# Optimization experiments

Measured on AMD Instinct MI355X. Metric: run time of the kernel, lower is better.

## Reference

```python
import jax, jax.numpy as jnp
import numpy as np

BETA = 0.9       # neuron_args['beta']
THRESH = 0.5     # neuron_args['threshold'] (mem_thresh)
ALPHA = 2.0      # surrogate.atan(alpha=2)
BIN = 50         # int(0.2 / 0.004)
NSTEPS = 7       # num_steps
STEP = BIN // NSTEPS  # 7 -> only buffer[:49] is used


@jax.custom_vjp
def atan_spike(x):
    return (x > 0).astype(x.dtype)

def _asp_fwd(x):
    return (x > 0).astype(x.dtype), x

def _asp_bwd(x, g):
    return (g * (ALPHA / 2.0) / (1.0 + (jnp.pi / 2.0 * ALPHA * x) ** 2),)

atan_spike.defvjp(_asp_fwd, _asp_bwd)


def _heaviside_detached(x):
    # snntorch mem_reset: reset = spike_grad(mem - thresh).detach()
    return jax.lax.stop_gradient((x > 0).astype(x.dtype))


def _forward(x, W_in, W_h0, W_out, v_x, v_y):
    T, B, D = x.shape
    H = W_in.shape[0]
    O = W_out.shape[0]
    vxy = jnp.concatenate([v_x, v_y])  # (2,)

    def single_forward(acc):  # acc: (NSTEPS, B, D)
        mem1 = jnp.zeros((B, H), x.dtype)
        mem2 = jnp.zeros((B, H), x.dtype)
        mem_out = jnp.zeros((B, O), x.dtype)
        for s in range(NSTEPS):
            cur = acc[s] @ W_in.T                      # (B, H); dropout in eval mode = identity
            reset = _heaviside_detached(mem1 - THRESH)
            mem1 = (BETA * mem1 + cur) * (1.0 - reset)  # reset_mechanism='zero'
            spk = atan_spike(mem1 - THRESH)
            cur = spk @ W_h0.T
            reset = _heaviside_detached(mem2 - THRESH)
            mem2 = (BETA * mem2 + cur) * (1.0 - reset)
            spk = atan_spike(mem2 - THRESH)
            cur = spk @ W_out.T                        # (B, O)
            mem_out = BETA * mem_out + cur             # reset_mechanism='none'
        return mem_out

    def step(carry, x_t):
        buf, L = carry  # buf: (BIN, B, D) zero-padded past L valid frames
        # torch: append then trim front when >BIN. While growing, frames keep
        # fixed positions with zeros at the end (NOT a sliding window yet).
        grow = jax.lax.dynamic_update_slice_in_dim(buf, x_t[None], L, 0)
        slide = jnp.concatenate([buf[1:], x_t[None]], axis=0)
        buf = jnp.where(L < BIN, grow, slide)
        L = jnp.minimum(L + 1, BIN)
        # acc_spikes[i] = sum(buf[7i : 7i+7]); frame 49 unused (49 = 7*7)
        acc = buf[: NSTEPS * STEP].reshape(NSTEPS, STEP, B, D).sum(axis=1)
        pred = single_forward(acc)                     # (B, 2)
        return (buf, L), pred * vxy

    init = (jnp.zeros((BIN, B, D), x.dtype), jnp.int32(1))  # one initial zero frame
    _, preds = jax.lax.scan(step, init, x)             # (T, B, 2)
    return preds


def setup_inputs() -> dict:
    key = jax.random.key(0)
    ks = jax.random.split(key, 6)
    T, B, D, H, O = 128, 1024, 96, 128, 2
    x = jax.random.uniform(ks[0], (T, B, D), dtype=jnp.float32)
    W_in = jax.random.normal(ks[1], (H, D), dtype=jnp.float32) / np.sqrt(D)
    W_h0 = jax.random.normal(ks[2], (H, H), dtype=jnp.float32) / np.sqrt(H)
    W_out = jax.random.normal(ks[3], (O, H), dtype=jnp.float32) / np.sqrt(H)
    v_x = jax.random.normal(ks[4], (1,), dtype=jnp.float32)
    v_y = jax.random.normal(ks[5], (1,), dtype=jnp.float32)
    return {"x": x, "W_in": W_in, "W_h0": W_h0, "W_out": W_out, "v_x": v_x, "v_y": v_y}


def reference(x, W_in, W_h0, W_out, v_x, v_y):
    return _forward(x, W_in, W_h0, W_out, v_x, v_y)
```

## Files before the change

kernel.cpp:

```cpp
#include <hip/hip_runtime.h>
#include <cstdint>

#define T_STEPS 128
#define BATCH   1024
#define D_INPUT 96
#define H_DIM   128
#define NWIN    163

__device__ __forceinline__ void win_decode(int widx, int& start, int& len) {
    if (widx < 121)      { start = widx;        len = 7; }
    else if (widx < 127) { start = 0;           len = widx - 120; }
    else { const int r = widx - 127; const int s = 1 + r / 6;
           len = 1 + r % 6;          start = 7 * s - 1; }
}

__device__ __forceinline__ int widx_for(int t, int s) {
    if (t >= 49) return t - 49 + 7 * s;
    if (s == 0)  return 121 + min(5, t);
    const int st = 7 * s - 1;
    if (t < st) return -1;
    const int len = min(7, t - st + 1);
    return (len == 7) ? st : (127 + (s - 1) * 6 + (len - 1));
}

__device__ __forceinline__ int swz_idx(int row, int col) {
    return (row << 7) | (col ^ ((row & 63) << 1));
}

__global__ __launch_bounds__(256) void kA_wincur(const float* __restrict__ x,
                                                 const float* __restrict__ Win,
                                                 float* __restrict__ CUR1) {
    __shared__ float xs[D_INPUT * 32];
    __shared__ float wT[D_INPUT * H_DIM];
    const int widx = blockIdx.x;
    const int b0   = blockIdx.y * 32;
    int start, len; win_decode(widx, start, len);
    const int tid = threadIdx.x;

    for (int e = tid; e < H_DIM * D_INPUT; e += 256) {
        const int h = e / D_INPUT, d = e % D_INPUT;
        wT[swz_idx(d, h)] = Win[e];
    }
    for (int e = tid; e < D_INPUT * 32; e += 256) {
        const int d = e % D_INPUT, bq = e / D_INPUT;
        const float* xp = x + ((size_t)start * BATCH + b0 + bq) * D_INPUT + d;
        float s = xp[0];
        for (int k = 1; k < len; ++k)
            s = __fadd_rn(s, xp[(size_t)k * BATCH * D_INPUT]);
        xs[d * 32 + bq] = s;
    }
    __syncthreads();

    const int hp = tid & 63, g = tid >> 6;
    const int h0 = hp << 1;
    float acc[8][2];
#pragma unroll
    for (int r = 0; r < 8; ++r) { acc[r][0] = 0.f; acc[r][1] = 0.f; }

#pragma unroll 6
    for (int d = 0; d < D_INPUT; ++d) {
        const float2 wp  = *(const float2*)&wT[swz_idx(d, h0)];
        const float4 xv0 = *(const float4*)&xs[d * 32 + g * 8];
        const float4 xv1 = *(const float4*)&xs[d * 32 + g * 8 + 4];
        const float xv[8] = {xv0.x,xv0.y,xv0.z,xv0.w, xv1.x,xv1.y,xv1.z,xv1.w};
#pragma unroll
        for (int r = 0; r < 8; ++r) {
            acc[r][0] = __fmaf_rn(xv[r], wp.x, acc[r][0]);
            acc[r][1] = __fmaf_rn(xv[r], wp.y, acc[r][1]);
        }
    }
    float* op = CUR1 + ((size_t)widx * BATCH + b0 + g * 8) * H_DIM + h0;
#pragma unroll
    for (int r = 0; r < 8; ++r) {
        float2 o; o.x = acc[r][0]; o.y = acc[r][1];
        *(float2*)(op + (size_t)r * H_DIM) = o;
    }
}

__global__ __launch_bounds__(512, 2) void kB_snn(const float* __restrict__ CUR1,
                                                 const float* __restrict__ Wh0,
                                                 const float* __restrict__ Wout,
                                                 const float* __restrict__ vxp,
                                                 const float* __restrict__ vyp,
                                                 float* __restrict__ out) {
    __shared__ float lw[H_DIM * H_DIM];
    __shared__ float sf[8][64 * 32];
    const int tid = threadIdx.x;
    for (int e = tid; e < H_DIM * H_DIM; e += 512) {
        const int i = e >> 7, h = e & 127;
        lw[swz_idx(h, i)] = Wh0[e];
    }
    __syncthreads();

    const int w = tid >> 6, lane = tid & 63;
    const int t  = blockIdx.y;
    const int i0 = lane << 1;
    float* sfw = sf[w];
    const int lbase = lane * 32;
    const float wex = Wout[i0],     wey = Wout[H_DIM + i0];
    const float wox = Wout[i0 + 1], woy = Wout[H_DIM + i0 + 1];
    const float vx = vxp[0], vy = vyp[0];
    const int b0 = (blockIdx.x << 7) + (w << 4);

    float m1a[16], m1b[16], m2a[16], m2b[16], poa[16], pob[16];
    float c1a[16], c1b[16];
    bool  s1a[16], s1b[16], s2a[16], s2b[16];
#pragma unroll
    for (int k = 0; k < 16; ++k) {
        m1a[k]=0.f; m1b[k]=0.f; m2a[k]=0.f; m2b[k]=0.f; poa[k]=0.f; pob[k]=0.f;
        s1a[k]=false; s1b[k]=false; s2a[k]=false; s2b[k]=false;
    }

    {
        const int wi = widx_for(t, 0);
#pragma unroll
        for (int k = 0; k < 16; ++k) {
            c1a[k] = 0.f; c1b[k] = 0.f;
            if (wi >= 0) {
                const float2 v = *(const float2*)
                    &CUR1[((size_t)wi * BATCH + b0 + k) * H_DIM + i0];
                c1a[k] = v.x; c1b[k] = v.y;
            }
        }
    }

#pragma unroll 1
    for (int s = 0; s < 7; ++s) {
        float sev[16], sov[16];
#pragma unroll
        for (int k = 0; k < 16; ++k) {
            m1a[k] = s1a[k] ? 0.f : __fadd_rn(__fmul_rn(0.9f, m1a[k]), c1a[k]);
            m1b[k] = s1b[k] ? 0.f : __fadd_rn(__fmul_rn(0.9f, m1b[k]), c1b[k]);
            s1a[k] = m1a[k] > 0.5f; s1b[k] = m1b[k] > 0.5f;
            sev[k] = s1a[k] ? 1.0f : 0.0f;
            sov[k] = s1b[k] ? 1.0f : 0.0f;
        }
#pragma unroll
        for (int c = 0; c < 4; ++c) {
            float4 v;
            v.x = sev[c*4]; v.y = sev[c*4+1]; v.z = sev[c*4+2]; v.w = sev[c*4+3];
            *(float4*)&sfw[lbase + ((c     ^ (lane & 7)) << 2)] = v;
            v.x = sov[c*4]; v.y = sov[c*4+1]; v.z = sov[c*4+2]; v.w = sov[c*4+3];
            *(float4*)&sfw[lbase + (((c+4) ^ (lane & 7)) << 2)] = v;
        }

        const int win = (s < 6) ? widx_for(t, s + 1) : -1;
#pragma unroll
        for (int k = 0; k < 16; ++k) {
            c1a[k] = 0.f; c1b[k] = 0.f;
            if (win >= 0) {
                const float2 v = *(const float2*)
                    &CUR1[((size_t)win * BATCH + b0 + k) * H_DIM + i0];
                c1a[k] = v.x; c1b[k] = v.y;
            }
        }

        float c2a[16], c2b[16];
#pragma unroll
        for (int k = 0; k < 16; ++k) { c2a[k] = 0.f; c2b[k] = 0.f; }
#pragma unroll 8
        for (int j = 0; j < 64; ++j) {
            const float2 we = *(const float2*)&lw[swz_idx(2*j,     i0)];
            const float2 wo = *(const float2*)&lw[swz_idx(2*j + 1, i0)];
            const int jb = j * 32, jx = (j & 7) << 2;
            const float4 e0 = *(const float4*)&sfw[jb + ((0  << 2) ^ jx)];
            const float4 e1 = *(const float4*)&sfw[jb + ((1  << 2) ^ jx)];
            const float4 e2 = *(const float4*)&sfw[jb + ((2  << 2) ^ jx)];
            const float4 e3 = *(const float4*)&sfw[jb + ((3  << 2) ^ jx)];
            const float4 o0 = *(const float4*)&sfw[jb + ((4  << 2) ^ jx)];
            const float4 o1 = *(const float4*)&sfw[jb + ((5  << 2) ^ jx)];
            const float4 o2 = *(const float4*)&sfw[jb + ((6  << 2) ^ jx)];
            const float4 o3 = *(const float4*)&sfw[jb + ((7  << 2) ^ jx)];
            const float se[16] = {e0.x,e0.y,e0.z,e0.w, e1.x,e1.y,e1.z,e1.w,
                                  e2.x,e2.y,e2.z,e2.w, e3.x,e3.y,e3.z,e3.w};
            const float so[16] = {o0.x,o0.y,o0.z,o0.w, o1.x,o1.y,o1.z,o1.w,
                                  o2.x,o2.y,o2.z,o2.w, o3.x,o3.y,o3.z,o3.w};
#pragma unroll
            for (int k = 0; k < 16; ++k) {
                c2a[k] = __fmaf_rn(se[k], we.x, c2a[k]);
                c2b[k] = __fmaf_rn(se[k], we.y, c2b[k]);
                c2a[k] = __fmaf_rn(so[k], wo.x, c2a[k]);
                c2b[k] = __fmaf_rn(so[k], wo.y, c2b[k]);
            }
        }

#pragma unroll
        for (int k = 0; k < 16; ++k) {
            m2a[k] = s2a[k] ? 0.f : __fadd_rn(__fmul_rn(0.9f, m2a[k]), c2a[k]);
            m2b[k] = s2b[k] ? 0.f : __fadd_rn(__fmul_rn(0.9f, m2b[k]), c2b[k]);
            s2a[k] = m2a[k] > 0.5f; s2b[k] = m2b[k] > 0.5f;
            const float p0 = (s2a[k] ? wex : 0.f) + (s2b[k] ? wox : 0.f);
            const float p1 = (s2a[k] ? wey : 0.f) + (s2b[k] ? woy : 0.f);
            poa[k] = __fmaf_rn(0.9f, poa[k], p0);
            pob[k] = __fmaf_rn(0.9f, pob[k], p1);
        }
    }

#pragma unroll
    for (int k = 0; k < 16; ++k) {
        float r0 = poa[k], r1 = pob[k];
#pragma unroll
        for (int off = 32; off > 0; off >>= 1) {
            r0 += __shfl_xor(r0, off);
            r1 += __shfl_xor(r1, off);
        }
        if (lane == 0) {
            float2 o;
            o.x = __fmul_rn(r0, vx);
            o.y = __fmul_rn(r1, vy);
            *(float2*)(out + ((size_t)t * BATCH + b0 + k) * 2) = o;
        }
    }
}

extern "C" void kernel_launch(void* const* d_in, const int* in_sizes, int n_in,
                              void* d_out, int out_size, void* d_ws, size_t ws_size,
                              hipStream_t stream) {
    const float* x    = (const float*)d_in[0];
    const float* Win  = (const float*)d_in[1];
    const float* Wh0  = (const float*)d_in[2];
    const float* Wout = (const float*)d_in[3];
    const float* vx   = (const float*)d_in[4];
    const float* vy   = (const float*)d_in[5];
    float* out  = (float*)d_out;
    float* CUR1 = (float*)d_ws;

    kA_wincur<<<dim3(NWIN, BATCH / 32),    dim3(256), 0, stream>>>(x, Win, CUR1);
    kB_snn   <<<dim3(BATCH / 128, T_STEPS), dim3(512), 0, stream>>>(CUR1, Wh0, Wout, vx, vy, out);
}
```

Before: 899.0 us.

## Precompute window sums and transposed W_in in separate pre-pass kernels

Adds a kernel that streams x once per element through a 7-entry register ring and writes every distinct window sum to workspace. It also adds a kernel that pre-transposes W_in. The window-current kernel now loads precomputed sums with a coalesced float2 weight copy instead of re-reading up to 7 strided frames and transposing W_in in every block. This trades repeated strided x reads and per-block transposes for an extra 163x1024x96 float write and read of the workspace plus two more launches.

```diff
diff --git a/kernel.cpp b/kernel.cpp
--- a/kernel.cpp
+++ b/kernel.cpp
@@ -6,13 +6,7 @@
 #define D_INPUT 96
 #define H_DIM   128
 #define NWIN    163
-
-__device__ __forceinline__ void win_decode(int widx, int& start, int& len) {
-    if (widx < 121)      { start = widx;        len = 7; }
-    else if (widx < 127) { start = 0;           len = widx - 120; }
-    else { const int r = widx - 127; const int s = 1 + r / 6;
-           len = 1 + r % 6;          start = 7 * s - 1; }
-}
+#define BD      (BATCH * D_INPUT)
 
 __device__ __forceinline__ int widx_for(int t, int s) {
     if (t >= 49) return t - 49 + 7 * s;
@@ -27,27 +21,67 @@
     return (row << 7) | (col ^ ((row & 63) << 1));
 }
 
-__global__ __launch_bounds__(256) void kA_wincur(const float* __restrict__ x,
-                                                 const float* __restrict__ Win,
+__global__ __launch_bounds__(256) void kT_wint(const float* __restrict__ Win,
+                                               float* __restrict__ WinT) {
+    const int e = blockIdx.x * 256 + threadIdx.x;
+    const int h = e / D_INPUT, d = e % D_INPUT;
+    WinT[d * H_DIM + h] = Win[e];
+}
+
+__global__ __launch_bounds__(256) void kA0_winsum(const float* __restrict__ x,
+                                                  float* __restrict__ WS) {
+    const int flat = blockIdx.x * 256 + threadIdx.x;
+    float* wsp = WS + flat;
+    float r[7];
+#pragma unroll
+    for (int t = 0; t < T_STEPS; ++t) {
+        r[t % 7] = x[(size_t)t * BD + flat];
+        if (t <= 5) {
+            float s = r[0];
+#pragma unroll
+            for (int k = 1; k <= t; ++k) s = __fadd_rn(s, r[k % 7]);
+            wsp[(size_t)(121 + t) * BD] = s;
+        }
+        if (t >= 6 && t <= 126) {
+            const int w = t - 6;
+            float s = r[w % 7];
+#pragma unroll
+            for (int k = 1; k < 7; ++k) s = __fadd_rn(s, r[(w + k) % 7]);
+            wsp[(size_t)w * BD] = s;
+        }
+        if (t >= 6 && t <= 46) {
+            const int sv = (t + 1) / 7;
+            if (sv >= 1 && 7 * sv >= t - 4 && 7 * sv <= t + 1) {
+                const int start = 7 * sv - 1;
+                const int len = t - start + 1;
+                float s = r[start % 7];
+#pragma unroll
+                for (int k = 1; k < len; ++k) s = __fadd_rn(s, r[(start + k) % 7]);
+                wsp[(size_t)(127 + (sv - 1) * 6 + (len - 1)) * BD] = s;
+            }
+        }
+    }
+}
+
+__global__ __launch_bounds__(256) void kA_wincur(const float* __restrict__ WS,
+                                                 const float* __restrict__ WinT,
                                                  float* __restrict__ CUR1) {
     __shared__ float xs[D_INPUT * 32];
     __shared__ float wT[D_INPUT * H_DIM];
     const int widx = blockIdx.x;
     const int b0   = blockIdx.y * 32;
-    int start, len; win_decode(widx, start, len);
-    const int tid = threadIdx.x;
-
-    for (int e = tid; e < H_DIM * D_INPUT; e += 256) {
-        const int h = e / D_INPUT, d = e % D_INPUT;
-        wT[swz_idx(d, h)] = Win[e];
+    const int tid  = threadIdx.x;
+
+    {
+        const float2* WinT2 = (const float2*)WinT;
+        for (int e2 = tid; e2 < D_INPUT * (H_DIM / 2); e2 += 256) {
+            const int d = e2 >> 6, h2 = e2 & 63;
+            *(float2*)&wT[swz_idx(d, h2 << 1)] = WinT2[e2];
+        }
     }
     for (int e = tid; e < D_INPUT * 32; e += 256) {
         const int d = e % D_INPUT, bq = e / D_INPUT;
-        const float* xp = x + ((size_t)start * BATCH + b0 + bq) * D_INPUT + d;
-        float s = xp[0];
-        for (int k = 1; k < len; ++k)
-            s = __fadd_rn(s, xp[(size_t)k * BATCH * D_INPUT]);
-        xs[d * 32 + bq] = s;
+        xs[d * 32 + bq] = WS[(size_t)widx * BD + (size_t)(b0 + bq) * D_INPUT + d];
     }
     __syncthreads();
 
@@ -223,8 +257,13 @@
     const float* vx   = (const float*)d_in[4];
     const float* vy   = (const float*)d_in[5];
     float* out  = (float*)d_out;
+
     float* CUR1 = (float*)d_ws;
-
-    kA_wincur<<<dim3(NWIN, BATCH / 32),    dim3(256), 0, stream>>>(x, Win, CUR1);
-    kB_snn   <<<dim3(BATCH / 128, T_STEPS), dim3(512), 0, stream>>>(CUR1, Wh0, Wout, vx, vy, out);
-}
+    float* WS   = CUR1 + (size_t)NWIN * BATCH * H_DIM;
+    float* WinT = WS   + (size_t)NWIN * BATCH * D_INPUT;
+
+    kT_wint  <<<dim3((H_DIM * D_INPUT) / 256), dim3(256), 0, stream>>>(Win, WinT);
+    kA0_winsum<<<dim3(BD / 256),               dim3(256), 0, stream>>>(x, WS);
+    kA_wincur<<<dim3(NWIN, BATCH / 32),        dim3(256), 0, stream>>>(WS, WinT, CUR1);
+    kB_snn   <<<dim3(BATCH / 128, T_STEPS),    dim3(512), 0, stream>>>(CUR1, Wh0, Wout, vx, vy, out);
+}
```

New measurement: 911.8 us. About the same (+1.4%).
